# Performance work log

Measured on AMD Instinct MI355X. Metric: run time of the kernel, lower is better.

The kernel has to match this reference:

```python
import jax, jax.numpy as jnp
import numpy as np

T, H, F, E, K = 4096, 2048, 1408, 8, 2  # tokens, hidden, intermediate, experts, top_k


def setup_inputs() -> dict:
    key = jax.random.key(0)
    k1, k2, k3, k4 = jax.random.split(key, 4)
    return {
        "hidden_states": jax.random.normal(k1, (T, H), dtype=jnp.float32),
        "router_logits": jax.random.normal(k2, (T, E), dtype=jnp.float32),
        # w1: (E, 2, H, F) where dim 1 = [gate_proj, up_proj]
        "w1": jax.random.normal(k3, (E, 2, H, F), dtype=jnp.float32) * 0.02,
        # w2: (E, F, H) down projection
        "w2": jax.random.normal(k4, (E, F, H), dtype=jnp.float32) * 0.02,
        "top_k": K,
    }


def reference(hidden_states, router_logits, w1, w2, top_k):
    # Router: softmax over all experts, then select top_k.
    # renormalize_topk_logits=False -> combine weights are the raw softmax probs.
    probs = jax.nn.softmax(router_logits, axis=-1)            # (T, E)
    topk_w, topk_ids = jax.lax.top_k(probs, top_k)            # (T, K) each

    num_experts = w1.shape[0]
    out = jnp.zeros_like(hidden_states)                       # (T, H)
    # Fixed small loop over experts (structurally distinct weight slices);
    # each expert's FFN is a dense GEMM over all tokens, masked by the
    # per-token combine coefficient (0 for tokens not routed to this expert).
    for e in range(num_experts):
        coef = jnp.sum(jnp.where(topk_ids == e, topk_w, 0.0), axis=-1)  # (T,)
        gate = hidden_states @ w1[e, 0]                       # (T, F)
        up = hidden_states @ w1[e, 1]                         # (T, F)
        h = jax.nn.silu(gate) * up                            # SwiGLU
        out = out + coef[:, None] * (h @ w2[e])               # (T, H)
    return out
```

## Files before the change

### kernel.cpp

```cpp
#include <hip/hip_runtime.h>
#include <stdint.h>

#define T_TOK 4096
#define HID   2048
#define FF    1408
#define NE    8
#define BUF   16384
#define NT1   (HID / 32)
#define NT2   (FF / 32)

typedef __attribute__((ext_vector_type(8))) short short8;
typedef __attribute__((ext_vector_type(4))) float f32x4;

__device__ inline unsigned short f2bf(float f) {
  uint32_t u = __builtin_bit_cast(uint32_t, f);
  u += 0x7fffu + ((u >> 16) & 1u);
  return (unsigned short)(u >> 16);
}

__device__ inline uint32_t cvt_pk(float a, float b) {
  uint32_t r;
  asm("v_cvt_pk_bf16_f32 %0, %1, %2" : "=v"(r) : "v"(a), "v"(b));
  return r;
}

__device__ inline void gload16(const void* g, void* l) {
  __builtin_amdgcn_global_load_lds(
      (const __attribute__((address_space(1))) unsigned int*)g,
      (__attribute__((address_space(3))) unsigned int*)l, 16, 0, 0);
}

__device__ inline void wait8_barrier() {
  asm volatile("s_waitcnt vmcnt(8)" ::: "memory");
  __builtin_amdgcn_s_barrier();
  asm volatile("" ::: "memory");
}
__device__ inline void wait4_barrier() {
  asm volatile("s_waitcnt vmcnt(4)" ::: "memory");
  __builtin_amdgcn_s_barrier();
  asm volatile("" ::: "memory");
}
__device__ inline void wait0_barrier() {
  asm volatile("s_waitcnt vmcnt(0)" ::: "memory");
  __builtin_amdgcn_s_barrier();
  asm volatile("" ::: "memory");
}

__global__ __launch_bounds__(256) void route_kernel(const float* __restrict__ logits,
                                                    int2* __restrict__ eids,
                                                    float2* __restrict__ ecfs) {
  int t = blockIdx.x * 256 + threadIdx.x;
  const float4* lp = (const float4*)(logits + (size_t)t * NE);
  float4 a = lp[0], b = lp[1];
  float l[8] = {a.x, a.y, a.z, a.w, b.x, b.y, b.z, b.w};
  float mx = l[0];
#pragma unroll
  for (int i = 1; i < 8; ++i) mx = fmaxf(mx, l[i]);
  float s = 0.f, p[8];
#pragma unroll
  for (int i = 0; i < 8; ++i) { p[i] = __expf(l[i] - mx); s += p[i]; }
  float inv = 1.f / s;
  int e0 = 0;
#pragma unroll
  for (int i = 1; i < 8; ++i) if (l[i] > l[e0]) e0 = i;
  int e1 = (e0 == 0) ? 1 : 0;
#pragma unroll
  for (int i = 0; i < 8; ++i) if (i != e0 && l[i] > l[e1]) e1 = i;
  eids[t] = make_int2(e0, e1);
  ecfs[t] = make_float2(p[e0] * inv, p[e1] * inv);
}

__global__ __launch_bounds__(256) void compact_kernel(const int2* __restrict__ eids,
                                                      const float2* __restrict__ ecfs,
                                                      int* __restrict__ tok,
                                                      float* __restrict__ coef,
                                                      int* __restrict__ rowptr,
                                                      int* __restrict__ invm) {
  int e = blockIdx.x, tid = threadIdx.x;
  __shared__ int hist[8];
  __shared__ int wsum[4];
  __shared__ int runv;
  if (tid < 8) hist[tid] = 0;
  __syncthreads();
  for (int t = tid; t < T_TOK; t += 256) {
    int2 ei = eids[t];
    atomicAdd(&hist[ei.x], 1);
    atomicAdd(&hist[ei.y], 1);
  }
  __syncthreads();
  int off = 0;
  for (int j = 0; j < e; ++j) off += hist[j];
  if (tid == 0) {
    runv = 0;
    if (e == 0) rowptr[0] = 0;
    rowptr[e + 1] = off + hist[e];
  }
  __syncthreads();
  int wave = tid >> 6, lane = tid & 63;
  for (int c = 0; c < T_TOK; c += 256) {
    int t = c + tid;
    int2 ei = eids[t];
    float2 cf = ecfs[t];
    bool fl = false; float cv = 0.f; int ks = 0;
    if (ei.x == e)      { fl = true; cv = cf.x; ks = 0; }
    else if (ei.y == e) { fl = true; cv = cf.y; ks = 1; }
    unsigned long long m = __ballot(fl);
    if (lane == 0) wsum[wave] = __popcll(m);
    __syncthreads();
    int woff = runv;
    for (int wv = 0; wv < wave; ++wv) woff += wsum[wv];
    int pos = off + woff + __popcll(m & ((1ull << lane) - 1ull));
    if (fl) { tok[pos] = t; coef[pos] = cv; invm[2 * t + ks] = pos; }
    __syncthreads();
    if (tid == 0) runv += wsum[0] + wsum[1] + wsum[2] + wsum[3];
    __syncthreads();
  }
}

__global__ __launch_bounds__(256) void cvtx_kernel(const float* __restrict__ x,
                                                   unsigned short* __restrict__ xb) {
  int i = blockIdx.x * 256 + threadIdx.x;
  float4 v = ((const float4*)x)[i];
  uint2 o;
  o.x = cvt_pk(v.x, v.y);
  o.y = cvt_pk(v.z, v.w);
  ((uint2*)xb)[i] = o;
}

__global__ __launch_bounds__(256) void wcvt_kernel(const float* __restrict__ in,
                                                   unsigned short* __restrict__ out,
                                                   int R, int C) {
  __shared__ unsigned short t[64][72];
  const float* ip = in + ((size_t)blockIdx.z * R + blockIdx.y * 64) * C + blockIdx.x * 64;
  int tid = threadIdx.x;
  int r = tid >> 2, cg = (tid & 3) * 16;
  const float* rp = ip + (size_t)r * C + cg;
#pragma unroll
  for (int j = 0; j < 4; ++j) {
    float4 v = *(const float4*)(rp + j * 4);
    int c = cg + j * 4;
    t[c + 0][r] = f2bf(v.x);
    t[c + 1][r] = f2bf(v.y);
    t[c + 2][r] = f2bf(v.z);
    t[c + 3][r] = f2bf(v.w);
  }
  __syncthreads();
  int cr = tid >> 2, kg = (tid & 3) * 16;
  unsigned short* op = out + ((size_t)blockIdx.z * C + blockIdx.x * 64 + cr) * R +
                       blockIdx.y * 64 + kg;
  *(short8*)op = *(const short8*)&t[cr][kg];
  *(short8*)(op + 8) = *(const short8*)&t[cr][kg + 8];
}

__global__ __launch_bounds__(256) void gemm1_kernel(const unsigned short* __restrict__ Xb,
                                                    const unsigned short* __restrict__ w1t,
                                                    const int* __restrict__ tok,
                                                    const int* __restrict__ rowptr,
                                                    unsigned short* __restrict__ hbuf) {
  int f = blockIdx.x + 22 * blockIdx.y;
  int g = (f & 7) * 88 + (f >> 3);
  int ftile = g >> 5, mtile = g & 31;
  int e = blockIdx.z;
  int base = rowptr[e], cnt = rowptr[e + 1] - base;
  if (mtile * 128 >= cnt) return;
  __shared__ char smem[4 * BUF];
  int tid = threadIdx.x, lane = tid & 63, wave = tid >> 6;

  int rA = wave * 32 + (lane >> 2);
  int cd = (lane & 3) ^ ((rA >> 1) & 3);
  int sA0 = min(mtile * 128 + rA, cnt - 1);
  int sA1 = min(mtile * 128 + rA + 16, cnt - 1);
  const unsigned short* gA0 = Xb + (size_t)tok[base + sA0] * HID + cd * 8;
  const unsigned short* gA1 = Xb + (size_t)tok[base + sA1] * HID + cd * 8;
  int r1 = rA + 16;
  int p0 = (rA >> 4) & 1, f0 = (rA & 15) + 16 * (rA >> 5);
  int p1 = (r1 >> 4) & 1, f1 = (r1 & 15) + 16 * (r1 >> 5);
  const unsigned short* gB0 = w1t + ((size_t)(e * 2 + p0) * FF + ftile * 64 + f0) * HID + cd * 8;
  const unsigned short* gB1 = w1t + ((size_t)(e * 2 + p1) * FF + ftile * 64 + f1) * HID + cd * 8;
  int lb = wave * 2048 + lane * 16;

#define STG1(bp, k0) do {                          \
    gload16(gA0 + (k0), (bp) + lb);                \
    gload16(gA1 + (k0), (bp) + lb + 1024);         \
    gload16(gB0 + (k0), (bp) + 8192 + lb);         \
    gload16(gB1 + (k0), (bp) + 8192 + lb + 1024);  \
  } while (0)

  int wm = wave >> 1, wn = wave & 1, kc = lane >> 4;
  int aoff[4], boff[4];
#pragma unroll
  for (int mi = 0; mi < 4; ++mi) {
    int row = wm * 64 + mi * 16 + (lane & 15);
    aoff[mi] = row * 64 + ((kc ^ ((row >> 1) & 3)) << 4);
  }
#pragma unroll
  for (int ni = 0; ni < 4; ++ni) {
    int n = wn * 64 + ni * 16 + (lane & 15);
    boff[ni] = 8192 + n * 64 + ((kc ^ ((n >> 1) & 3)) << 4);
  }

  const f32x4 vz = {0.f, 0.f, 0.f, 0.f};
  f32x4 acc[4][4];
#pragma unroll
  for (int mi = 0; mi < 4; ++mi)
#pragma unroll
    for (int ni = 0; ni < 4; ++ni) acc[mi][ni] = vz;

  STG1(smem, 0);
  STG1(smem + BUF, 32);
  STG1(smem + 2 * BUF, 64);
  wait8_barrier();

  for (int t = 0; t < NT1; ++t) {
    char* cur = smem + (t & 3) * BUF;
    bool pf = (t + 3) < NT1;
    if (pf) STG1(smem + ((t + 3) & 3) * BUF, (t + 3) * 32);
    short8 af[4], bb[4];
#pragma unroll
    for (int mi = 0; mi < 4; ++mi) af[mi] = *(const short8*)(cur + aoff[mi]);
#pragma unroll
    for (int ni = 0; ni < 4; ++ni) bb[ni] = *(const short8*)(cur + boff[ni]);
    __builtin_amdgcn_s_setprio(1);
#pragma unroll
    for (int mi = 0; mi < 4; ++mi)
#pragma unroll
      for (int ni = 0; ni < 4; ++ni)
        acc[mi][ni] = __builtin_amdgcn_mfma_f32_16x16x32_bf16(af[mi], bb[ni], acc[mi][ni], 0, 0, 0);
    __builtin_amdgcn_s_setprio(0);
    if (pf) wait8_barrier();
    else if (t + 2 < NT1) wait4_barrier();
    else wait0_barrier();
  }
#undef STG1

  int fb = ftile * 64 + wn * 32 + (lane & 15);
#pragma unroll
  for (int mi = 0; mi < 4; ++mi) {
#pragma unroll
    for (int i = 0; i < 4; ++i) {
      int ml = wm * 64 + mi * 16 + (lane >> 4) * 4 + i;
      int slot = mtile * 128 + ml;
      if (slot < cnt) {
        size_t hrow = (size_t)(base + slot) * FF + fb;
        float g0 = acc[mi][0][i], u0 = acc[mi][1][i];
        float g1 = acc[mi][2][i], u1 = acc[mi][3][i];
        hbuf[hrow]      = f2bf(g0 / (1.f + __expf(-g0)) * u0);
        hbuf[hrow + 16] = f2bf(g1 / (1.f + __expf(-g1)) * u1);
      }
    }
  }
}

__global__ __launch_bounds__(256) void gemm2_kernel(const unsigned short* __restrict__ hbuf,
                                                    const unsigned short* __restrict__ w2t,
                                                    const int* __restrict__ rowptr,
                                                    float* __restrict__ obuf) {
  int f = blockIdx.x + 16 * blockIdx.y;
  int g = (f & 7) * 64 + (f >> 3);
  int ntile = g >> 5, mtile = g & 31;
  int e = blockIdx.z;
  int base = rowptr[e], cnt = rowptr[e + 1] - base;
  if (mtile * 128 >= cnt) return;
  __shared__ char smem[3 * BUF];
  int tid = threadIdx.x, lane = tid & 63, wave = tid >> 6;

  int rA = wave * 32 + (lane >> 2);
  int cd = (lane & 3) ^ ((rA >> 1) & 3);
  int sA0 = min(mtile * 128 + rA, cnt - 1);
  int sA1 = min(mtile * 128 + rA + 16, cnt - 1);
  const unsigned short* gA0 = hbuf + (size_t)(base + sA0) * FF + cd * 8;
  const unsigned short* gA1 = hbuf + (size_t)(base + sA1) * FF + cd * 8;
  const unsigned short* gB0 = w2t + ((size_t)e * HID + ntile * 128 + rA) * FF + cd * 8;
  const unsigned short* gB1 = gB0 + (size_t)16 * FF;
  int lb = wave * 2048 + lane * 16;

#define STG2(bp, k0) do {                          \
    gload16(gA0 + (k0), (bp) + lb);                \
    gload16(gA1 + (k0), (bp) + lb + 1024);         \
    gload16(gB0 + (k0), (bp) + 8192 + lb);         \
    gload16(gB1 + (k0), (bp) + 8192 + lb + 1024);  \
  } while (0)

  int wm = wave >> 1, wn = wave & 1, kc = lane >> 4;
  int aoff[4], boff[4];
#pragma unroll
  for (int mi = 0; mi < 4; ++mi) {
    int row = wm * 64 + mi * 16 + (lane & 15);
    aoff[mi] = row * 64 + ((kc ^ ((row >> 1) & 3)) << 4);
  }
#pragma unroll
  for (int ni = 0; ni < 4; ++ni) {
    int n = wn * 64 + ni * 16 + (lane & 15);
    boff[ni] = 8192 + n * 64 + ((kc ^ ((n >> 1) & 3)) << 4);
  }

  const f32x4 vz = {0.f, 0.f, 0.f, 0.f};
  f32x4 acc[4][4];
#pragma unroll
  for (int mi = 0; mi < 4; ++mi)
#pragma unroll
    for (int ni = 0; ni < 4; ++ni) acc[mi][ni] = vz;

  STG2(smem, 0);
  STG2(smem + BUF, 32);
  wait4_barrier();

  char* cur = smem;
  char* nxt = smem + 2 * BUF;
  for (int t = 0; t < NT2; ++t) {
    bool pf = (t + 2) < NT2;
    if (pf) STG2(nxt, (t + 2) * 32);
    short8 af[4], bb[4];
#pragma unroll
    for (int mi = 0; mi < 4; ++mi) af[mi] = *(const short8*)(cur + aoff[mi]);
#pragma unroll
    for (int ni = 0; ni < 4; ++ni) bb[ni] = *(const short8*)(cur + boff[ni]);
    __builtin_amdgcn_s_setprio(1);
#pragma unroll
    for (int mi = 0; mi < 4; ++mi)
#pragma unroll
      for (int ni = 0; ni < 4; ++ni)
        acc[mi][ni] = __builtin_amdgcn_mfma_f32_16x16x32_bf16(af[mi], bb[ni], acc[mi][ni], 0, 0, 0);
    __builtin_amdgcn_s_setprio(0);
    if (pf) wait4_barrier(); else wait0_barrier();
    cur = (cur == smem + 2 * BUF) ? smem : cur + BUF;
    nxt = (nxt == smem + 2 * BUF) ? smem : nxt + BUF;
  }
#undef STG2

  int nb = ntile * 128 + wn * 64 + (lane & 15);
#pragma unroll
  for (int mi = 0; mi < 4; ++mi) {
#pragma unroll
    for (int i = 0; i < 4; ++i) {
      int ml = wm * 64 + mi * 16 + (lane >> 4) * 4 + i;
      int slot = mtile * 128 + ml;
      if (slot < cnt) {
        float* op = obuf + (size_t)(base + slot) * HID + nb;
#pragma unroll
        for (int ni = 0; ni < 4; ++ni) op[ni * 16] = acc[mi][ni][i];
      }
    }
  }
}

__global__ __launch_bounds__(256) void combine_kernel(const float* __restrict__ obuf,
                                                      const int2* __restrict__ invm,
                                                      const float* __restrict__ coef,
                                                      float* __restrict__ out) {
  int idx = blockIdx.x * 256 + threadIdx.x;
  int t = idx >> 9, h4 = idx & 511;
  int2 pp = invm[t];
  float c0 = coef[pp.x], c1 = coef[pp.y];
  float4 a = ((const float4*)(obuf + (size_t)pp.x * HID))[h4];
  float4 b = ((const float4*)(obuf + (size_t)pp.y * HID))[h4];
  float4 o;
  o.x = c0 * a.x + c1 * b.x;
  o.y = c0 * a.y + c1 * b.y;
  o.z = c0 * a.z + c1 * b.z;
  o.w = c0 * a.w + c1 * b.w;
  ((float4*)out)[idx] = o;
}

__global__ __launch_bounds__(256) void gemm2_atomic(const unsigned short* __restrict__ hbuf,
                                                    const unsigned short* __restrict__ w2t,
                                                    const int* __restrict__ tok,
                                                    const float* __restrict__ coef,
                                                    const int* __restrict__ rowptr,
                                                    float* __restrict__ out) {
  int f = blockIdx.x + 16 * blockIdx.y;
  int g = (f & 7) * 64 + (f >> 3);
  int ntile = g >> 5, mtile = g & 31;
  int e = blockIdx.z;
  int base = rowptr[e], cnt = rowptr[e + 1] - base;
  if (mtile * 128 >= cnt) return;
  __shared__ char smem[3 * BUF];
  __shared__ int tokL[128];
  __shared__ float cofL[128];
  int tid = threadIdx.x, lane = tid & 63, wave = tid >> 6;
  if (tid < 128) {
    int slot = min(mtile * 128 + tid, cnt - 1);
    tokL[tid] = tok[base + slot];
    cofL[tid] = coef[base + slot];
  }
  __syncthreads();

  int rA = wave * 32 + (lane >> 2);
  int cd = (lane & 3) ^ ((rA >> 1) & 3);
  int sA0 = min(mtile * 128 + rA, cnt - 1);
  int sA1 = min(mtile * 128 + rA + 16, cnt - 1);
  const unsigned short* gA0 = hbuf + (size_t)(base + sA0) * FF + cd * 8;
  const unsigned short* gA1 = hbuf + (size_t)(base + sA1) * FF + cd * 8;
  const unsigned short* gB0 = w2t + ((size_t)e * HID + ntile * 128 + rA) * FF + cd * 8;
  const unsigned short* gB1 = gB0 + (size_t)16 * FF;
  int lb = wave * 2048 + lane * 16;

#define STG2F(bp, k0) do {                         \
    gload16(gA0 + (k0), (bp) + lb);                \
    gload16(gA1 + (k0), (bp) + lb + 1024);         \
    gload16(gB0 + (k0), (bp) + 8192 + lb);         \
    gload16(gB1 + (k0), (bp) + 8192 + lb + 1024);  \
  } while (0)

  int wm = wave >> 1, wn = wave & 1, kc = lane >> 4;
  int aoff[4], boff[4];
#pragma unroll
  for (int mi = 0; mi < 4; ++mi) {
    int row = wm * 64 + mi * 16 + (lane & 15);
    aoff[mi] = row * 64 + ((kc ^ ((row >> 1) & 3)) << 4);
  }
#pragma unroll
  for (int ni = 0; ni < 4; ++ni) {
    int n = wn * 64 + ni * 16 + (lane & 15);
    boff[ni] = 8192 + n * 64 + ((kc ^ ((n >> 1) & 3)) << 4);
  }

  const f32x4 vz = {0.f, 0.f, 0.f, 0.f};
  f32x4 acc[4][4];
#pragma unroll
  for (int mi = 0; mi < 4; ++mi)
#pragma unroll
    for (int ni = 0; ni < 4; ++ni) acc[mi][ni] = vz;

  STG2F(smem, 0);
  STG2F(smem + BUF, 32);
  wait4_barrier();

  char* cur = smem;
  char* nxt = smem + 2 * BUF;
  for (int t = 0; t < NT2; ++t) {
    bool pf = (t + 2) < NT2;
    if (pf) STG2F(nxt, (t + 2) * 32);
    short8 af[4], bb[4];
#pragma unroll
    for (int mi = 0; mi < 4; ++mi) af[mi] = *(const short8*)(cur + aoff[mi]);
#pragma unroll
    for (int ni = 0; ni < 4; ++ni) bb[ni] = *(const short8*)(cur + boff[ni]);
    __builtin_amdgcn_s_setprio(1);
#pragma unroll
    for (int mi = 0; mi < 4; ++mi)
#pragma unroll
      for (int ni = 0; ni < 4; ++ni)
        acc[mi][ni] = __builtin_amdgcn_mfma_f32_16x16x32_bf16(af[mi], bb[ni], acc[mi][ni], 0, 0, 0);
    __builtin_amdgcn_s_setprio(0);
    if (pf) wait4_barrier(); else wait0_barrier();
    cur = (cur == smem + 2 * BUF) ? smem : cur + BUF;
    nxt = (nxt == smem + 2 * BUF) ? smem : nxt + BUF;
  }
#undef STG2F

#pragma unroll
  for (int mi = 0; mi < 4; ++mi) {
#pragma unroll
    for (int i = 0; i < 4; ++i) {
      int ml = wm * 64 + mi * 16 + (lane >> 4) * 4 + i;
      int slot = mtile * 128 + ml;
      if (slot < cnt) {
        float cf = cofL[ml];
        float* op = out + (size_t)tokL[ml] * HID + ntile * 128 + wn * 64 + (lane & 15);
#pragma unroll
        for (int ni = 0; ni < 4; ++ni)
          unsafeAtomicAdd(op + ni * 16, cf * acc[mi][ni][i]);
      }
    }
  }
}

extern "C" void kernel_launch(void* const* d_in, const int* in_sizes, int n_in,
                              void* d_out, int out_size, void* d_ws, size_t ws_size,
                              hipStream_t stream) {
  const float* X  = (const float*)d_in[0];
  const float* RL = (const float*)d_in[1];
  const float* W1 = (const float*)d_in[2];
  const float* W2 = (const float*)d_in[3];
  float* out = (float*)d_out;

  const size_t OFF_EIDS = 4096;
  const size_t OFF_ECFS = 36864;
  const size_t OFF_TOK  = 69632;
  const size_t OFF_COEF = 102400;
  const size_t OFF_XB   = 135168;
  const size_t OFF_H    = 16912384;
  const size_t OFF_W1T  = 39981056;
  const size_t OFF_W2T  = 132255744;
  const size_t TOTAL2   = 178393088;
  const size_t OFF_INV  = 178393088;
  const size_t TOTAL3   = 178425856;
  if (ws_size < TOTAL2 || n_in < 4) return;
  bool big = ws_size >= TOTAL3;

  char* w = (char*)d_ws;
  int*    rowptr = (int*)w;
  int2*   eids   = (int2*)(w + OFF_EIDS);
  float2* ecfs   = (float2*)(w + OFF_ECFS);
  int*    tok    = (int*)(w + OFF_TOK);
  float*  coef   = (float*)(w + OFF_COEF);
  unsigned short* Xb   = (unsigned short*)(w + OFF_XB);
  unsigned short* hbuf = (unsigned short*)(w + OFF_H);
  unsigned short* w1t  = (unsigned short*)(w + OFF_W1T);
  unsigned short* w2t  = (unsigned short*)(w + OFF_W2T);
  float* obuf = (float*)(w + OFF_W1T);
  int* invm = big ? (int*)(w + OFF_INV) : (int*)hbuf;

  if (!big) hipMemsetAsync(d_out, 0, (size_t)T_TOK * HID * sizeof(float), stream);
  route_kernel<<<T_TOK / 256, 256, 0, stream>>>(RL, eids, ecfs);
  compact_kernel<<<NE, 256, 0, stream>>>(eids, ecfs, tok, coef, rowptr, invm);
  cvtx_kernel<<<(T_TOK * HID / 4) / 256, 256, 0, stream>>>(X, Xb);
  wcvt_kernel<<<dim3(FF / 64, HID / 64, NE * 2), 256, 0, stream>>>(W1, w1t, HID, FF);
  wcvt_kernel<<<dim3(HID / 64, FF / 64, NE), 256, 0, stream>>>(W2, w2t, FF, HID);
  gemm1_kernel<<<dim3(FF / 64, T_TOK / 128, NE), 256, 0, stream>>>(Xb, w1t, tok, rowptr, hbuf);
  if (big) {
    gemm2_kernel<<<dim3(HID / 128, T_TOK / 128, NE), 256, 0, stream>>>(hbuf, w2t, rowptr, obuf);
    combine_kernel<<<(T_TOK * HID / 4) / 256, 256, 0, stream>>>(obuf, (const int2*)invm, coef, out);
  } else {
    gemm2_atomic<<<dim3(HID / 128, T_TOK / 128, NE), 256, 0, stream>>>(hbuf, w2t, tok, coef, rowptr, out);
  }
}
```

Measured before the change: 345.6 us.

## Enlarge GEMM tiles to 128x256, fuse routing into compaction, store bf16 partials

Both expert GEMMs now use 128x256 output tiles with triple-buffered LDS, and each wave holds a 4x8 MFMA accumulator grid instead of 4x4, giving more reuse per loaded tile. The separate routing kernel is removed and each compaction block recomputes softmax/top-2 inline. GEMM2 writes its per-expert partial outputs as bf16 rather than fp32, so the combine kernel reads half the bytes. The larger tiles raise register and LDS pressure and may lower occupancy. The bf16 intermediate adds rounding error to the output.

Result: slower. 375.6 us (+8.7%).

```diff
diff --git a/kernel.cpp b/kernel.cpp
--- a/kernel.cpp
+++ b/kernel.cpp
@@ -5,9 +5,10 @@
 #define HID   2048
 #define FF    1408
 #define NE    8
-#define BUF   16384
+#define BUF   24576
 #define NT1   (HID / 32)
 #define NT2   (FF / 32)
+#define OBUF  16384
 
 typedef __attribute__((ext_vector_type(8))) short short8;
 typedef __attribute__((ext_vector_type(4))) float f32x4;
@@ -17,7 +18,10 @@
   u += 0x7fffu + ((u >> 16) & 1u);
   return (unsigned short)(u >> 16);
 }
-
+__device__ inline float bf2f(unsigned short u) {
+  uint32_t x = ((uint32_t)u) << 16;
+  return __builtin_bit_cast(float, x);
+}
 __device__ inline uint32_t cvt_pk(float a, float b) {
   uint32_t r;
   asm("v_cvt_pk_bf16_f32 %0, %1, %2" : "=v"(r) : "v"(a), "v"(b));
@@ -30,8 +34,8 @@
       (__attribute__((address_space(3))) unsigned int*)l, 16, 0, 0);
 }
 
-__device__ inline void wait8_barrier() {
-  asm volatile("s_waitcnt vmcnt(8)" ::: "memory");
+__device__ inline void wait6_barrier() {
+  asm volatile("s_waitcnt vmcnt(6)" ::: "memory");
   __builtin_amdgcn_s_barrier();
   asm volatile("" ::: "memory");
 }
@@ -46,12 +50,9 @@
   asm volatile("" ::: "memory");
 }
 
-__global__ __launch_bounds__(256) void route_kernel(const float* __restrict__ logits,
-                                                    int2* __restrict__ eids,
-                                                    float2* __restrict__ ecfs) {
-  int t = blockIdx.x * 256 + threadIdx.x;
-  const float4* lp = (const float4*)(logits + (size_t)t * NE);
-  float4 a = lp[0], b = lp[1];
+__device__ inline void route1(const float* __restrict__ lp, int& e0, int& e1,
+                              float& c0, float& c1) {
+  float4 a = ((const float4*)lp)[0], b = ((const float4*)lp)[1];
   float l[8] = {a.x, a.y, a.z, a.w, b.x, b.y, b.z, b.w};
   float mx = l[0];
 #pragma unroll
@@ -60,18 +61,17 @@
 #pragma unroll
   for (int i = 0; i < 8; ++i) { p[i] = __expf(l[i] - mx); s += p[i]; }
   float inv = 1.f / s;
-  int e0 = 0;
+  e0 = 0;
 #pragma unroll
   for (int i = 1; i < 8; ++i) if (l[i] > l[e0]) e0 = i;
-  int e1 = (e0 == 0) ? 1 : 0;
+  e1 = (e0 == 0) ? 1 : 0;
 #pragma unroll
   for (int i = 0; i < 8; ++i) if (i != e0 && l[i] > l[e1]) e1 = i;
-  eids[t] = make_int2(e0, e1);
-  ecfs[t] = make_float2(p[e0] * inv, p[e1] * inv);
-}
-
-__global__ __launch_bounds__(256) void compact_kernel(const int2* __restrict__ eids,
-                                                      const float2* __restrict__ ecfs,
+  c0 = p[e0] * inv;
+  c1 = p[e1] * inv;
+}
+
+__global__ __launch_bounds__(256) void compact_kernel(const float* __restrict__ logits,
                                                       int* __restrict__ tok,
                                                       float* __restrict__ coef,
                                                       int* __restrict__ rowptr,
@@ -83,9 +83,10 @@
   if (tid < 8) hist[tid] = 0;
   __syncthreads();
   for (int t = tid; t < T_TOK; t += 256) {
-    int2 ei = eids[t];
-    atomicAdd(&hist[ei.x], 1);
-    atomicAdd(&hist[ei.y], 1);
+    int e0, e1; float c0, c1;
+    route1(logits + (size_t)t * NE, e0, e1, c0, c1);
+    atomicAdd(&hist[e0], 1);
+    atomicAdd(&hist[e1], 1);
   }
   __syncthreads();
   int off = 0;
@@ -99,11 +100,11 @@
   int wave = tid >> 6, lane = tid & 63;
   for (int c = 0; c < T_TOK; c += 256) {
     int t = c + tid;
-    int2 ei = eids[t];
-    float2 cf = ecfs[t];
+    int e0, e1; float c0, c1;
+    route1(logits + (size_t)t * NE, e0, e1, c0, c1);
     bool fl = false; float cv = 0.f; int ks = 0;
-    if (ei.x == e)      { fl = true; cv = cf.x; ks = 0; }
-    else if (ei.y == e) { fl = true; cv = cf.y; ks = 1; }
+    if (e0 == e)      { fl = true; cv = c0; ks = 0; }
+    else if (e1 == e) { fl = true; cv = c1; ks = 1; }
     unsigned long long m = __ballot(fl);
     if (lane == 0) wsum[wave] = __popcll(m);
     __syncthreads();
@@ -152,214 +153,223 @@
   *(short8*)(op + 8) = *(const short8*)&t[cr][kg + 8];
 }
 
-__global__ __launch_bounds__(256) void gemm1_kernel(const unsigned short* __restrict__ Xb,
-                                                    const unsigned short* __restrict__ w1t,
-                                                    const int* __restrict__ tok,
-                                                    const int* __restrict__ rowptr,
-                                                    unsigned short* __restrict__ hbuf) {
-  int f = blockIdx.x + 22 * blockIdx.y;
-  int g = (f & 7) * 88 + (f >> 3);
+__global__ __launch_bounds__(256, 2) void gemm1_kernel(const unsigned short* __restrict__ Xb,
+                                                       const unsigned short* __restrict__ w1t,
+                                                       const int* __restrict__ tok,
+                                                       const int* __restrict__ rowptr,
+                                                       unsigned short* __restrict__ hbuf) {
+  int e = blockIdx.z;
+  int f = blockIdx.x + 32 * blockIdx.y;
+  int g = (f & 7) * 44 + (f >> 3);
   int ftile = g >> 5, mtile = g & 31;
-  int e = blockIdx.z;
-  int base = rowptr[e], cnt = rowptr[e + 1] - base;
-  if (mtile * 128 >= cnt) return;
-  __shared__ char smem[4 * BUF];
-  int tid = threadIdx.x, lane = tid & 63, wave = tid >> 6;
-
-  int rA = wave * 32 + (lane >> 2);
-  int cd = (lane & 3) ^ ((rA >> 1) & 3);
-  int sA0 = min(mtile * 128 + rA, cnt - 1);
-  int sA1 = min(mtile * 128 + rA + 16, cnt - 1);
-  const unsigned short* gA0 = Xb + (size_t)tok[base + sA0] * HID + cd * 8;
-  const unsigned short* gA1 = Xb + (size_t)tok[base + sA1] * HID + cd * 8;
-  int r1 = rA + 16;
-  int p0 = (rA >> 4) & 1, f0 = (rA & 15) + 16 * (rA >> 5);
-  int p1 = (r1 >> 4) & 1, f1 = (r1 & 15) + 16 * (r1 >> 5);
-  const unsigned short* gB0 = w1t + ((size_t)(e * 2 + p0) * FF + ftile * 64 + f0) * HID + cd * 8;
-  const unsigned short* gB1 = w1t + ((size_t)(e * 2 + p1) * FF + ftile * 64 + f1) * HID + cd * 8;
-  int lb = wave * 2048 + lane * 16;
-
-#define STG1(bp, k0) do {                          \
-    gload16(gA0 + (k0), (bp) + lb);                \
-    gload16(gA1 + (k0), (bp) + lb + 1024);         \
-    gload16(gB0 + (k0), (bp) + 8192 + lb);         \
-    gload16(gB1 + (k0), (bp) + 8192 + lb + 1024);  \
-  } while (0)
-
-  int wm = wave >> 1, wn = wave & 1, kc = lane >> 4;
-  int aoff[4], boff[4];
-#pragma unroll
-  for (int mi = 0; mi < 4; ++mi) {
-    int row = wm * 64 + mi * 16 + (lane & 15);
-    aoff[mi] = row * 64 + ((kc ^ ((row >> 1) & 3)) << 4);
-  }
-#pragma unroll
-  for (int ni = 0; ni < 4; ++ni) {
-    int n = wn * 64 + ni * 16 + (lane & 15);
-    boff[ni] = 8192 + n * 64 + ((kc ^ ((n >> 1) & 3)) << 4);
-  }
-
-  const f32x4 vz = {0.f, 0.f, 0.f, 0.f};
-  f32x4 acc[4][4];
-#pragma unroll
-  for (int mi = 0; mi < 4; ++mi)
-#pragma unroll
-    for (int ni = 0; ni < 4; ++ni) acc[mi][ni] = vz;
-
-  STG1(smem, 0);
-  STG1(smem + BUF, 32);
-  STG1(smem + 2 * BUF, 64);
-  wait8_barrier();
-
-  for (int t = 0; t < NT1; ++t) {
-    char* cur = smem + (t & 3) * BUF;
-    bool pf = (t + 3) < NT1;
-    if (pf) STG1(smem + ((t + 3) & 3) * BUF, (t + 3) * 32);
-    short8 af[4], bb[4];
-#pragma unroll
-    for (int mi = 0; mi < 4; ++mi) af[mi] = *(const short8*)(cur + aoff[mi]);
-#pragma unroll
-    for (int ni = 0; ni < 4; ++ni) bb[ni] = *(const short8*)(cur + boff[ni]);
-    __builtin_amdgcn_s_setprio(1);
-#pragma unroll
-    for (int mi = 0; mi < 4; ++mi)
-#pragma unroll
-      for (int ni = 0; ni < 4; ++ni)
-        acc[mi][ni] = __builtin_amdgcn_mfma_f32_16x16x32_bf16(af[mi], bb[ni], acc[mi][ni], 0, 0, 0);
-    __builtin_amdgcn_s_setprio(0);
-    if (pf) wait8_barrier();
-    else if (t + 2 < NT1) wait4_barrier();
-    else wait0_barrier();
-  }
-#undef STG1
-
-  int fb = ftile * 64 + wn * 32 + (lane & 15);
-#pragma unroll
-  for (int mi = 0; mi < 4; ++mi) {
-#pragma unroll
-    for (int i = 0; i < 4; ++i) {
-      int ml = wm * 64 + mi * 16 + (lane >> 4) * 4 + i;
-      int slot = mtile * 128 + ml;
-      if (slot < cnt) {
-        size_t hrow = (size_t)(base + slot) * FF + fb;
-        float g0 = acc[mi][0][i], u0 = acc[mi][1][i];
-        float g1 = acc[mi][2][i], u1 = acc[mi][3][i];
-        hbuf[hrow]      = f2bf(g0 / (1.f + __expf(-g0)) * u0);
-        hbuf[hrow + 16] = f2bf(g1 / (1.f + __expf(-g1)) * u1);
-      }
-    }
-  }
-}
-
-__global__ __launch_bounds__(256) void gemm2_kernel(const unsigned short* __restrict__ hbuf,
-                                                    const unsigned short* __restrict__ w2t,
-                                                    const int* __restrict__ rowptr,
-                                                    float* __restrict__ obuf) {
-  int f = blockIdx.x + 16 * blockIdx.y;
-  int g = (f & 7) * 64 + (f >> 3);
-  int ntile = g >> 5, mtile = g & 31;
-  int e = blockIdx.z;
   int base = rowptr[e], cnt = rowptr[e + 1] - base;
   if (mtile * 128 >= cnt) return;
   __shared__ char smem[3 * BUF];
   int tid = threadIdx.x, lane = tid & 63, wave = tid >> 6;
 
-  int rA = wave * 32 + (lane >> 2);
-  int cd = (lane & 3) ^ ((rA >> 1) & 3);
-  int sA0 = min(mtile * 128 + rA, cnt - 1);
-  int sA1 = min(mtile * 128 + rA + 16, cnt - 1);
+  int q = tid >> 2, p = tid & 3;
+  int cd = p ^ ((q >> 1) & 3);
+  int sA0 = min(mtile * 128 + q, cnt - 1);
+  int sA1 = min(mtile * 128 + 64 + q, cnt - 1);
+  const unsigned short* gA0 = Xb + (size_t)tok[base + sA0] * HID + cd * 8;
+  const unsigned short* gA1 = Xb + (size_t)tok[base + sA1] * HID + cd * 8;
+  const unsigned short* gB[4];
+#pragma unroll
+  for (int c = 0; c < 4; ++c) {
+    int row = 64 * c + q;
+    int proj = (row >> 4) & 1;
+    int fg = ftile * 128 + (row & 15) + 16 * (row >> 5);
+    gB[c] = w1t + ((size_t)(e * 2 + proj) * FF + fg) * HID + cd * 8;
+  }
+  int ldst = tid * 16;
+
+#define STG1(bp, k0) do {                                   \
+    gload16(gA0 + (k0), (bp) + ldst);                       \
+    gload16(gA1 + (k0), (bp) + 4096 + ldst);                \
+    _Pragma("unroll") for (int c = 0; c < 4; ++c)           \
+      gload16(gB[c] + (k0), (bp) + 8192 + c * 4096 + ldst); \
+  } while (0)
+
+  int wm = wave >> 1, wn = wave & 1, kc = lane >> 4, j = lane & 15;
+  int aoff[4], boff[8];
+#pragma unroll
+  for (int mi = 0; mi < 4; ++mi) {
+    int row = wm * 64 + mi * 16 + j;
+    aoff[mi] = row * 64 + ((kc ^ ((row >> 1) & 3)) << 4);
+  }
+#pragma unroll
+  for (int ni = 0; ni < 8; ++ni) {
+    int brow = wn * 128 + ni * 16 + j;
+    boff[ni] = 8192 + brow * 64 + ((kc ^ ((brow >> 1) & 3)) << 4);
+  }
+
+  const f32x4 vz = {0.f, 0.f, 0.f, 0.f};
+  f32x4 acc[4][8];
+#pragma unroll
+  for (int mi = 0; mi < 4; ++mi)
+#pragma unroll
+    for (int ni = 0; ni < 8; ++ni) acc[mi][ni] = vz;
+
+  STG1(smem, 0);
+  STG1(smem + BUF, 32);
+  wait6_barrier();
+
+  for (int t = 0; t < NT1; ++t) {
+    char* cur = smem + (t % 3) * BUF;
+    bool pf = (t + 2) < NT1;
+    if (pf) STG1(smem + ((t + 2) % 3) * BUF, (t + 2) * 32);
+    short8 af[4], bb[8];
+#pragma unroll
+    for (int mi = 0; mi < 4; ++mi) af[mi] = *(const short8*)(cur + aoff[mi]);
+#pragma unroll
+    for (int ni = 0; ni < 8; ++ni) bb[ni] = *(const short8*)(cur + boff[ni]);
+    __builtin_amdgcn_s_setprio(1);
+#pragma unroll
+    for (int mi = 0; mi < 4; ++mi)
+#pragma unroll
+      for (int ni = 0; ni < 8; ++ni)
+        acc[mi][ni] = __builtin_amdgcn_mfma_f32_16x16x32_bf16(af[mi], bb[ni], acc[mi][ni], 0, 0, 0);
+    __builtin_amdgcn_s_setprio(0);
+    if (pf) wait6_barrier(); else wait0_barrier();
+  }
+#undef STG1
+
+  int gq = lane >> 4;
+#pragma unroll
+  for (int mi = 0; mi < 4; ++mi) {
+#pragma unroll
+    for (int i = 0; i < 4; ++i) {
+      int ml = wm * 64 + mi * 16 + gq * 4 + i;
+      int slot = mtile * 128 + ml;
+      if (slot < cnt) {
+        size_t hrow = (size_t)(base + slot) * FF;
+#pragma unroll
+        for (int qd = 0; qd < 4; ++qd) {
+          int fg = ftile * 128 + j + 16 * (wn * 4 + qd);
+          float gg = acc[mi][2 * qd][i], uu = acc[mi][2 * qd + 1][i];
+          float hv = gg / (1.f + __expf(-gg)) * uu;
+          hbuf[hrow + fg] = f2bf(hv);
+        }
+      }
+    }
+  }
+}
+
+__global__ __launch_bounds__(256, 2) void gemm2_kernel(const unsigned short* __restrict__ hbuf,
+                                                       const unsigned short* __restrict__ w2t,
+                                                       const int* __restrict__ rowptr,
+                                                       unsigned short* __restrict__ obuf) {
+  int e = blockIdx.z;
+  int f = blockIdx.x + 32 * blockIdx.y;
+  int g = (f & 7) * 32 + (f >> 3);
+  int ntile = g >> 5, mtile = g & 31;
+  int base = rowptr[e], cnt = rowptr[e + 1] - base;
+  if (mtile * 128 >= cnt) return;
+  __shared__ char smem[3 * BUF];
+  int tid = threadIdx.x, lane = tid & 63, wave = tid >> 6;
+
+  int q = tid >> 2, p = tid & 3;
+  int cd = p ^ ((q >> 1) & 3);
+  int sA0 = min(mtile * 128 + q, cnt - 1);
+  int sA1 = min(mtile * 128 + 64 + q, cnt - 1);
   const unsigned short* gA0 = hbuf + (size_t)(base + sA0) * FF + cd * 8;
   const unsigned short* gA1 = hbuf + (size_t)(base + sA1) * FF + cd * 8;
-  const unsigned short* gB0 = w2t + ((size_t)e * HID + ntile * 128 + rA) * FF + cd * 8;
-  const unsigned short* gB1 = gB0 + (size_t)16 * FF;
-  int lb = wave * 2048 + lane * 16;
-
-#define STG2(bp, k0) do {                          \
-    gload16(gA0 + (k0), (bp) + lb);                \
-    gload16(gA1 + (k0), (bp) + lb + 1024);         \
-    gload16(gB0 + (k0), (bp) + 8192 + lb);         \
-    gload16(gB1 + (k0), (bp) + 8192 + lb + 1024);  \
+  const unsigned short* gB[4];
+#pragma unroll
+  for (int c = 0; c < 4; ++c)
+    gB[c] = w2t + ((size_t)e * HID + ntile * 256 + 64 * c + q) * FF + cd * 8;
+  int ldst = tid * 16;
+
+#define STG2(bp, k0) do {                                   \
+    gload16(gA0 + (k0), (bp) + ldst);                       \
+    gload16(gA1 + (k0), (bp) + 4096 + ldst);                \
+    _Pragma("unroll") for (int c = 0; c < 4; ++c)           \
+      gload16(gB[c] + (k0), (bp) + 8192 + c * 4096 + ldst); \
   } while (0)
 
-  int wm = wave >> 1, wn = wave & 1, kc = lane >> 4;
-  int aoff[4], boff[4];
+  int wm = wave >> 1, wn = wave & 1, kc = lane >> 4, j = lane & 15;
+  int aoff[4], boff[8];
 #pragma unroll
   for (int mi = 0; mi < 4; ++mi) {
-    int row = wm * 64 + mi * 16 + (lane & 15);
+    int row = wm * 64 + mi * 16 + j;
     aoff[mi] = row * 64 + ((kc ^ ((row >> 1) & 3)) << 4);
   }
 #pragma unroll
-  for (int ni = 0; ni < 4; ++ni) {
-    int n = wn * 64 + ni * 16 + (lane & 15);
-    boff[ni] = 8192 + n * 64 + ((kc ^ ((n >> 1) & 3)) << 4);
+  for (int ni = 0; ni < 8; ++ni) {
+    int brow = wn * 128 + ni * 16 + j;
+    boff[ni] = 8192 + brow * 64 + ((kc ^ ((brow >> 1) & 3)) << 4);
   }
 
   const f32x4 vz = {0.f, 0.f, 0.f, 0.f};
-  f32x4 acc[4][4];
+  f32x4 acc[4][8];
 #pragma unroll
   for (int mi = 0; mi < 4; ++mi)
 #pragma unroll
-    for (int ni = 0; ni < 4; ++ni) acc[mi][ni] = vz;
+    for (int ni = 0; ni < 8; ++ni) acc[mi][ni] = vz;
 
   STG2(smem, 0);
   STG2(smem + BUF, 32);
-  wait4_barrier();
-
-  char* cur = smem;
-  char* nxt = smem + 2 * BUF;
+  wait6_barrier();
+
   for (int t = 0; t < NT2; ++t) {
+    char* cur = smem + (t % 3) * BUF;
     bool pf = (t + 2) < NT2;
-    if (pf) STG2(nxt, (t + 2) * 32);
-    short8 af[4], bb[4];
+    if (pf) STG2(smem + ((t + 2) % 3) * BUF, (t + 2) * 32);
+    short8 af[4], bb[8];
 #pragma unroll
     for (int mi = 0; mi < 4; ++mi) af[mi] = *(const short8*)(cur + aoff[mi]);
 #pragma unroll
-    for (int ni = 0; ni < 4; ++ni) bb[ni] = *(const short8*)(cur + boff[ni]);
+    for (int ni = 0; ni < 8; ++ni) bb[ni] = *(const short8*)(cur + boff[ni]);
     __builtin_amdgcn_s_setprio(1);
 #pragma unroll
     for (int mi = 0; mi < 4; ++mi)
 #pragma unroll
-      for (int ni = 0; ni < 4; ++ni)
+      for (int ni = 0; ni < 8; ++ni)
         acc[mi][ni] = __builtin_amdgcn_mfma_f32_16x16x32_bf16(af[mi], bb[ni], acc[mi][ni], 0, 0, 0);
     __builtin_amdgcn_s_setprio(0);
-    if (pf) wait4_barrier(); else wait0_barrier();
-    cur = (cur == smem + 2 * BUF) ? smem : cur + BUF;
-    nxt = (nxt == smem + 2 * BUF) ? smem : nxt + BUF;
+    if (pf) wait6_barrier(); else wait0_barrier();
   }
 #undef STG2
 
-  int nb = ntile * 128 + wn * 64 + (lane & 15);
+  int gq = lane >> 4;
 #pragma unroll
   for (int mi = 0; mi < 4; ++mi) {
 #pragma unroll
     for (int i = 0; i < 4; ++i) {
-      int ml = wm * 64 + mi * 16 + (lane >> 4) * 4 + i;
+      int ml = wm * 64 + mi * 16 + gq * 4 + i;
       int slot = mtile * 128 + ml;
       if (slot < cnt) {
-        float* op = obuf + (size_t)(base + slot) * HID + nb;
-#pragma unroll
-        for (int ni = 0; ni < 4; ++ni) op[ni * 16] = acc[mi][ni][i];
+        unsigned short* op = obuf + (size_t)(base + slot) * HID + ntile * 256 +
+                             wn * 128 + j;
+#pragma unroll
+        for (int ni = 0; ni < 8; ++ni) op[ni * 16] = f2bf(acc[mi][ni][i]);
       }
     }
   }
 }
 
-__global__ __launch_bounds__(256) void combine_kernel(const float* __restrict__ obuf,
+__global__ __launch_bounds__(256) void combine_kernel(const unsigned short* __restrict__ obuf,
                                                       const int2* __restrict__ invm,
                                                       const float* __restrict__ coef,
                                                       float* __restrict__ out) {
   int idx = blockIdx.x * 256 + threadIdx.x;
-  int t = idx >> 9, h4 = idx & 511;
+  int t = idx >> 8, h8 = (idx & 255) * 8;
   int2 pp = invm[t];
   float c0 = coef[pp.x], c1 = coef[pp.y];
-  float4 a = ((const float4*)(obuf + (size_t)pp.x * HID))[h4];
-  float4 b = ((const float4*)(obuf + (size_t)pp.y * HID))[h4];
-  float4 o;
-  o.x = c0 * a.x + c1 * b.x;
-  o.y = c0 * a.y + c1 * b.y;
-  o.z = c0 * a.z + c1 * b.z;
-  o.w = c0 * a.w + c1 * b.w;
-  ((float4*)out)[idx] = o;
+  short8 a = *(const short8*)(obuf + (size_t)pp.x * HID + h8);
+  short8 b = *(const short8*)(obuf + (size_t)pp.y * HID + h8);
+  float4 o0, o1;
+  o0.x = c0 * bf2f((unsigned short)a[0]) + c1 * bf2f((unsigned short)b[0]);
+  o0.y = c0 * bf2f((unsigned short)a[1]) + c1 * bf2f((unsigned short)b[1]);
+  o0.z = c0 * bf2f((unsigned short)a[2]) + c1 * bf2f((unsigned short)b[2]);
+  o0.w = c0 * bf2f((unsigned short)a[3]) + c1 * bf2f((unsigned short)b[3]);
+  o1.x = c0 * bf2f((unsigned short)a[4]) + c1 * bf2f((unsigned short)b[4]);
+  o1.y = c0 * bf2f((unsigned short)a[5]) + c1 * bf2f((unsigned short)b[5]);
+  o1.z = c0 * bf2f((unsigned short)a[6]) + c1 * bf2f((unsigned short)b[6]);
+  o1.w = c0 * bf2f((unsigned short)a[7]) + c1 * bf2f((unsigned short)b[7]);
+  float4* ob = (float4*)(out + (size_t)t * HID + h8);
+  ob[0] = o0;
+  ob[1] = o1;
 }
 
 __global__ __launch_bounds__(256) void gemm2_atomic(const unsigned short* __restrict__ hbuf,
@@ -374,7 +384,7 @@
   int e = blockIdx.z;
   int base = rowptr[e], cnt = rowptr[e + 1] - base;
   if (mtile * 128 >= cnt) return;
-  __shared__ char smem[3 * BUF];
+  __shared__ char smem[3 * OBUF];
   __shared__ int tokL[128];
   __shared__ float cofL[128];
   int tid = threadIdx.x, lane = tid & 63, wave = tid >> 6;
@@ -423,11 +433,11 @@
     for (int ni = 0; ni < 4; ++ni) acc[mi][ni] = vz;
 
   STG2F(smem, 0);
-  STG2F(smem + BUF, 32);
+  STG2F(smem + OBUF, 32);
   wait4_barrier();
 
   char* cur = smem;
-  char* nxt = smem + 2 * BUF;
+  char* nxt = smem + 2 * OBUF;
   for (int t = 0; t < NT2; ++t) {
     bool pf = (t + 2) < NT2;
     if (pf) STG2F(nxt, (t + 2) * 32);
@@ -444,8 +454,8 @@
         acc[mi][ni] = __builtin_amdgcn_mfma_f32_16x16x32_bf16(af[mi], bb[ni], acc[mi][ni], 0, 0, 0);
     __builtin_amdgcn_s_setprio(0);
     if (pf) wait4_barrier(); else wait0_barrier();
-    cur = (cur == smem + 2 * BUF) ? smem : cur + BUF;
-    nxt = (nxt == smem + 2 * BUF) ? smem : nxt + BUF;
+    cur = (cur == smem + 2 * OBUF) ? smem : cur + OBUF;
+    nxt = (nxt == smem + 2 * OBUF) ? smem : nxt + OBUF;
   }
 #undef STG2F
 
@@ -475,8 +485,6 @@
   const float* W2 = (const float*)d_in[3];
   float* out = (float*)d_out;
 
-  const size_t OFF_EIDS = 4096;
-  const size_t OFF_ECFS = 36864;
   const size_t OFF_TOK  = 69632;
   const size_t OFF_COEF = 102400;
   const size_t OFF_XB   = 135168;
@@ -491,27 +499,24 @@
 
   char* w = (char*)d_ws;
   int*    rowptr = (int*)w;
-  int2*   eids   = (int2*)(w + OFF_EIDS);
-  float2* ecfs   = (float2*)(w + OFF_ECFS);
   int*    tok    = (int*)(w + OFF_TOK);
   float*  coef   = (float*)(w + OFF_COEF);
   unsigned short* Xb   = (unsigned short*)(w + OFF_XB);
   unsigned short* hbuf = (unsigned short*)(w + OFF_H);
   unsigned short* w1t  = (unsigned short*)(w + OFF_W1T);
   unsigned short* w2t  = (unsigned short*)(w + OFF_W2T);
-  float* obuf = (float*)(w + OFF_W1T);
+  unsigned short* obuf = (unsigned short*)(w + OFF_W1T);
   int* invm = big ? (int*)(w + OFF_INV) : (int*)hbuf;
 
   if (!big) hipMemsetAsync(d_out, 0, (size_t)T_TOK * HID * sizeof(float), stream);
-  route_kernel<<<T_TOK / 256, 256, 0, stream>>>(RL, eids, ecfs);
-  compact_kernel<<<NE, 256, 0, stream>>>(eids, ecfs, tok, coef, rowptr, invm);
+  compact_kernel<<<NE, 256, 0, stream>>>(RL, tok, coef, rowptr, invm);
   cvtx_kernel<<<(T_TOK * HID / 4) / 256, 256, 0, stream>>>(X, Xb);
   wcvt_kernel<<<dim3(FF / 64, HID / 64, NE * 2), 256, 0, stream>>>(W1, w1t, HID, FF);
   wcvt_kernel<<<dim3(HID / 64, FF / 64, NE), 256, 0, stream>>>(W2, w2t, FF, HID);
-  gemm1_kernel<<<dim3(FF / 64, T_TOK / 128, NE), 256, 0, stream>>>(Xb, w1t, tok, rowptr, hbuf);
+  gemm1_kernel<<<dim3(32, 11, NE), 256, 0, stream>>>(Xb, w1t, tok, rowptr, hbuf);
   if (big) {
-    gemm2_kernel<<<dim3(HID / 128, T_TOK / 128, NE), 256, 0, stream>>>(hbuf, w2t, rowptr, obuf);
-    combine_kernel<<<(T_TOK * HID / 4) / 256, 256, 0, stream>>>(obuf, (const int2*)invm, coef, out);
+    gemm2_kernel<<<dim3(32, 8, NE), 256, 0, stream>>>(hbuf, w2t, rowptr, obuf);
+    combine_kernel<<<(T_TOK * HID / 8) / 256, 256, 0, stream>>>(obuf, (const int2*)invm, coef, out);
   } else {
     gemm2_atomic<<<dim3(HID / 128, T_TOK / 128, NE), 256, 0, stream>>>(hbuf, w2t, tok, coef, rowptr, out);
   }
```

## Fuse routing into compaction, merge weight converts, bf16 expert outputs, interleave expert blocks

Applied to the files above, without the earlier changes.

Drops the separate route kernel and recomputes softmax/top-2 inside the compaction kernel. The two weight-transpose launches become a single launch. GEMM1 and GEMM2 switch to a 1D grid with experts interleaved across consecutive blocks. The per-expert GEMM2 output buffer is stored as bf16 instead of fp32, halving the write and combine-read traffic at some precision cost, and combine reads 8 bf16 values per thread.

Result: slower. 369.0 us (+6.8%).

```diff
diff --git a/kernel.cpp b/kernel.cpp
--- a/kernel.cpp
+++ b/kernel.cpp
@@ -17,7 +17,10 @@
   u += 0x7fffu + ((u >> 16) & 1u);
   return (unsigned short)(u >> 16);
 }
-
+__device__ inline float bf2f(unsigned short u) {
+  uint32_t x = ((uint32_t)u) << 16;
+  return __builtin_bit_cast(float, x);
+}
 __device__ inline uint32_t cvt_pk(float a, float b) {
   uint32_t r;
   asm("v_cvt_pk_bf16_f32 %0, %1, %2" : "=v"(r) : "v"(a), "v"(b));
@@ -46,12 +49,9 @@
   asm volatile("" ::: "memory");
 }
 
-__global__ __launch_bounds__(256) void route_kernel(const float* __restrict__ logits,
-                                                    int2* __restrict__ eids,
-                                                    float2* __restrict__ ecfs) {
-  int t = blockIdx.x * 256 + threadIdx.x;
-  const float4* lp = (const float4*)(logits + (size_t)t * NE);
-  float4 a = lp[0], b = lp[1];
+__device__ inline void route1(const float* __restrict__ lp, int& e0, int& e1,
+                              float& c0, float& c1) {
+  float4 a = ((const float4*)lp)[0], b = ((const float4*)lp)[1];
   float l[8] = {a.x, a.y, a.z, a.w, b.x, b.y, b.z, b.w};
   float mx = l[0];
 #pragma unroll
@@ -60,18 +60,17 @@
 #pragma unroll
   for (int i = 0; i < 8; ++i) { p[i] = __expf(l[i] - mx); s += p[i]; }
   float inv = 1.f / s;
-  int e0 = 0;
+  e0 = 0;
 #pragma unroll
   for (int i = 1; i < 8; ++i) if (l[i] > l[e0]) e0 = i;
-  int e1 = (e0 == 0) ? 1 : 0;
+  e1 = (e0 == 0) ? 1 : 0;
 #pragma unroll
   for (int i = 0; i < 8; ++i) if (i != e0 && l[i] > l[e1]) e1 = i;
-  eids[t] = make_int2(e0, e1);
-  ecfs[t] = make_float2(p[e0] * inv, p[e1] * inv);
-}
-
-__global__ __launch_bounds__(256) void compact_kernel(const int2* __restrict__ eids,
-                                                      const float2* __restrict__ ecfs,
+  c0 = p[e0] * inv;
+  c1 = p[e1] * inv;
+}
+
+__global__ __launch_bounds__(256) void compact_kernel(const float* __restrict__ logits,
                                                       int* __restrict__ tok,
                                                       float* __restrict__ coef,
                                                       int* __restrict__ rowptr,
@@ -83,9 +82,10 @@
   if (tid < 8) hist[tid] = 0;
   __syncthreads();
   for (int t = tid; t < T_TOK; t += 256) {
-    int2 ei = eids[t];
-    atomicAdd(&hist[ei.x], 1);
-    atomicAdd(&hist[ei.y], 1);
+    int e0, e1; float c0, c1;
+    route1(logits + (size_t)t * NE, e0, e1, c0, c1);
+    atomicAdd(&hist[e0], 1);
+    atomicAdd(&hist[e1], 1);
   }
   __syncthreads();
   int off = 0;
@@ -99,11 +99,11 @@
   int wave = tid >> 6, lane = tid & 63;
   for (int c = 0; c < T_TOK; c += 256) {
     int t = c + tid;
-    int2 ei = eids[t];
-    float2 cf = ecfs[t];
+    int e0, e1; float c0, c1;
+    route1(logits + (size_t)t * NE, e0, e1, c0, c1);
     bool fl = false; float cv = 0.f; int ks = 0;
-    if (ei.x == e)      { fl = true; cv = cf.x; ks = 0; }
-    else if (ei.y == e) { fl = true; cv = cf.y; ks = 1; }
+    if (e0 == e)      { fl = true; cv = c0; ks = 0; }
+    else if (e1 == e) { fl = true; cv = c1; ks = 1; }
     unsigned long long m = __ballot(fl);
     if (lane == 0) wsum[wave] = __popcll(m);
     __syncthreads();
@@ -127,11 +127,17 @@
   ((uint2*)xb)[i] = o;
 }
 
-__global__ __launch_bounds__(256) void wcvt_kernel(const float* __restrict__ in,
-                                                   unsigned short* __restrict__ out,
-                                                   int R, int C) {
+__global__ __launch_bounds__(256) void wcvt_all(const float* __restrict__ W1,
+                                                const float* __restrict__ W2,
+                                                unsigned short* __restrict__ w1t,
+                                                unsigned short* __restrict__ w2t) {
+  int z = blockIdx.z;
+  const float* in; unsigned short* out; int R, C;
+  if (z < 16) { in = W1 + (size_t)z * HID * FF;        out = w1t + (size_t)z * FF * HID;        R = HID; C = FF; }
+  else        { in = W2 + (size_t)(z - 16) * FF * HID; out = w2t + (size_t)(z - 16) * HID * FF; R = FF;  C = HID; }
+  if (blockIdx.x * 64 >= C || blockIdx.y * 64 >= R) return;
   __shared__ unsigned short t[64][72];
-  const float* ip = in + ((size_t)blockIdx.z * R + blockIdx.y * 64) * C + blockIdx.x * 64;
+  const float* ip = in + ((size_t)blockIdx.y * 64) * C + blockIdx.x * 64;
   int tid = threadIdx.x;
   int r = tid >> 2, cg = (tid & 3) * 16;
   const float* rp = ip + (size_t)r * C + cg;
@@ -146,8 +152,7 @@
   }
   __syncthreads();
   int cr = tid >> 2, kg = (tid & 3) * 16;
-  unsigned short* op = out + ((size_t)blockIdx.z * C + blockIdx.x * 64 + cr) * R +
-                       blockIdx.y * 64 + kg;
+  unsigned short* op = out + ((size_t)(blockIdx.x * 64 + cr)) * R + blockIdx.y * 64 + kg;
   *(short8*)op = *(const short8*)&t[cr][kg];
   *(short8*)(op + 8) = *(const short8*)&t[cr][kg + 8];
 }
@@ -157,10 +162,10 @@
                                                     const int* __restrict__ tok,
                                                     const int* __restrict__ rowptr,
                                                     unsigned short* __restrict__ hbuf) {
-  int f = blockIdx.x + 22 * blockIdx.y;
-  int g = (f & 7) * 88 + (f >> 3);
-  int ftile = g >> 5, mtile = g & 31;
-  int e = blockIdx.z;
+  int bid = blockIdx.x;
+  int e = bid & 7;
+  int i = bid >> 3;
+  int mtile = i & 31, ftile = i >> 5;
   int base = rowptr[e], cnt = rowptr[e + 1] - base;
   if (mtile * 128 >= cnt) return;
   __shared__ char smem[4 * BUF];
@@ -237,13 +242,13 @@
 #pragma unroll
   for (int mi = 0; mi < 4; ++mi) {
 #pragma unroll
-    for (int i = 0; i < 4; ++i) {
-      int ml = wm * 64 + mi * 16 + (lane >> 4) * 4 + i;
+    for (int i2 = 0; i2 < 4; ++i2) {
+      int ml = wm * 64 + mi * 16 + (lane >> 4) * 4 + i2;
       int slot = mtile * 128 + ml;
       if (slot < cnt) {
         size_t hrow = (size_t)(base + slot) * FF + fb;
-        float g0 = acc[mi][0][i], u0 = acc[mi][1][i];
-        float g1 = acc[mi][2][i], u1 = acc[mi][3][i];
+        float g0 = acc[mi][0][i2], u0 = acc[mi][1][i2];
+        float g1 = acc[mi][2][i2], u1 = acc[mi][3][i2];
         hbuf[hrow]      = f2bf(g0 / (1.f + __expf(-g0)) * u0);
         hbuf[hrow + 16] = f2bf(g1 / (1.f + __expf(-g1)) * u1);
       }
@@ -254,11 +259,11 @@
 __global__ __launch_bounds__(256) void gemm2_kernel(const unsigned short* __restrict__ hbuf,
                                                     const unsigned short* __restrict__ w2t,
                                                     const int* __restrict__ rowptr,
-                                                    float* __restrict__ obuf) {
-  int f = blockIdx.x + 16 * blockIdx.y;
-  int g = (f & 7) * 64 + (f >> 3);
-  int ntile = g >> 5, mtile = g & 31;
-  int e = blockIdx.z;
+                                                    unsigned short* __restrict__ obuf) {
+  int bid = blockIdx.x;
+  int e = bid & 7;
+  int i = bid >> 3;
+  int mtile = i & 31, ntile = i >> 5;
   int base = rowptr[e], cnt = rowptr[e + 1] - base;
   if (mtile * 128 >= cnt) return;
   __shared__ char smem[3 * BUF];
@@ -332,34 +337,40 @@
 #pragma unroll
   for (int mi = 0; mi < 4; ++mi) {
 #pragma unroll
-    for (int i = 0; i < 4; ++i) {
-      int ml = wm * 64 + mi * 16 + (lane >> 4) * 4 + i;
+    for (int i2 = 0; i2 < 4; ++i2) {
+      int ml = wm * 64 + mi * 16 + (lane >> 4) * 4 + i2;
       int slot = mtile * 128 + ml;
       if (slot < cnt) {
-        float* op = obuf + (size_t)(base + slot) * HID + nb;
-#pragma unroll
-        for (int ni = 0; ni < 4; ++ni) op[ni * 16] = acc[mi][ni][i];
+        unsigned short* op = obuf + (size_t)(base + slot) * HID + nb;
+#pragma unroll
+        for (int ni = 0; ni < 4; ++ni) op[ni * 16] = f2bf(acc[mi][ni][i2]);
       }
     }
   }
 }
 
-__global__ __launch_bounds__(256) void combine_kernel(const float* __restrict__ obuf,
+__global__ __launch_bounds__(256) void combine_kernel(const unsigned short* __restrict__ obuf,
                                                       const int2* __restrict__ invm,
                                                       const float* __restrict__ coef,
                                                       float* __restrict__ out) {
   int idx = blockIdx.x * 256 + threadIdx.x;
-  int t = idx >> 9, h4 = idx & 511;
+  int t = idx >> 8, h8 = (idx & 255) * 8;
   int2 pp = invm[t];
   float c0 = coef[pp.x], c1 = coef[pp.y];
-  float4 a = ((const float4*)(obuf + (size_t)pp.x * HID))[h4];
-  float4 b = ((const float4*)(obuf + (size_t)pp.y * HID))[h4];
-  float4 o;
-  o.x = c0 * a.x + c1 * b.x;
-  o.y = c0 * a.y + c1 * b.y;
-  o.z = c0 * a.z + c1 * b.z;
-  o.w = c0 * a.w + c1 * b.w;
-  ((float4*)out)[idx] = o;
+  short8 a = *(const short8*)(obuf + (size_t)pp.x * HID + h8);
+  short8 b = *(const short8*)(obuf + (size_t)pp.y * HID + h8);
+  float4 o0, o1;
+  o0.x = c0 * bf2f((unsigned short)a[0]) + c1 * bf2f((unsigned short)b[0]);
+  o0.y = c0 * bf2f((unsigned short)a[1]) + c1 * bf2f((unsigned short)b[1]);
+  o0.z = c0 * bf2f((unsigned short)a[2]) + c1 * bf2f((unsigned short)b[2]);
+  o0.w = c0 * bf2f((unsigned short)a[3]) + c1 * bf2f((unsigned short)b[3]);
+  o1.x = c0 * bf2f((unsigned short)a[4]) + c1 * bf2f((unsigned short)b[4]);
+  o1.y = c0 * bf2f((unsigned short)a[5]) + c1 * bf2f((unsigned short)b[5]);
+  o1.z = c0 * bf2f((unsigned short)a[6]) + c1 * bf2f((unsigned short)b[6]);
+  o1.w = c0 * bf2f((unsigned short)a[7]) + c1 * bf2f((unsigned short)b[7]);
+  float4* ob = (float4*)(out + (size_t)t * HID + h8);
+  ob[0] = o0;
+  ob[1] = o1;
 }
 
 __global__ __launch_bounds__(256) void gemm2_atomic(const unsigned short* __restrict__ hbuf,
@@ -452,15 +463,15 @@
 #pragma unroll
   for (int mi = 0; mi < 4; ++mi) {
 #pragma unroll
-    for (int i = 0; i < 4; ++i) {
-      int ml = wm * 64 + mi * 16 + (lane >> 4) * 4 + i;
+    for (int i2 = 0; i2 < 4; ++i2) {
+      int ml = wm * 64 + mi * 16 + (lane >> 4) * 4 + i2;
       int slot = mtile * 128 + ml;
       if (slot < cnt) {
         float cf = cofL[ml];
         float* op = out + (size_t)tokL[ml] * HID + ntile * 128 + wn * 64 + (lane & 15);
 #pragma unroll
         for (int ni = 0; ni < 4; ++ni)
-          unsafeAtomicAdd(op + ni * 16, cf * acc[mi][ni][i]);
+          unsafeAtomicAdd(op + ni * 16, cf * acc[mi][ni][i2]);
       }
     }
   }
@@ -475,8 +486,6 @@
   const float* W2 = (const float*)d_in[3];
   float* out = (float*)d_out;
 
-  const size_t OFF_EIDS = 4096;
-  const size_t OFF_ECFS = 36864;
   const size_t OFF_TOK  = 69632;
   const size_t OFF_COEF = 102400;
   const size_t OFF_XB   = 135168;
@@ -491,27 +500,23 @@
 
   char* w = (char*)d_ws;
   int*    rowptr = (int*)w;
-  int2*   eids   = (int2*)(w + OFF_EIDS);
-  float2* ecfs   = (float2*)(w + OFF_ECFS);
   int*    tok    = (int*)(w + OFF_TOK);
   float*  coef   = (float*)(w + OFF_COEF);
   unsigned short* Xb   = (unsigned short*)(w + OFF_XB);
   unsigned short* hbuf = (unsigned short*)(w + OFF_H);
   unsigned short* w1t  = (unsigned short*)(w + OFF_W1T);
   unsigned short* w2t  = (unsigned short*)(w + OFF_W2T);
-  float* obuf = (float*)(w + OFF_W1T);
+  unsigned short* obuf = (unsigned short*)(w + OFF_W1T);
   int* invm = big ? (int*)(w + OFF_INV) : (int*)hbuf;
 
   if (!big) hipMemsetAsync(d_out, 0, (size_t)T_TOK * HID * sizeof(float), stream);
-  route_kernel<<<T_TOK / 256, 256, 0, stream>>>(RL, eids, ecfs);
-  compact_kernel<<<NE, 256, 0, stream>>>(eids, ecfs, tok, coef, rowptr, invm);
+  compact_kernel<<<NE, 256, 0, stream>>>(RL, tok, coef, rowptr, invm);
   cvtx_kernel<<<(T_TOK * HID / 4) / 256, 256, 0, stream>>>(X, Xb);
-  wcvt_kernel<<<dim3(FF / 64, HID / 64, NE * 2), 256, 0, stream>>>(W1, w1t, HID, FF);
-  wcvt_kernel<<<dim3(HID / 64, FF / 64, NE), 256, 0, stream>>>(W2, w2t, FF, HID);
-  gemm1_kernel<<<dim3(FF / 64, T_TOK / 128, NE), 256, 0, stream>>>(Xb, w1t, tok, rowptr, hbuf);
+  wcvt_all<<<dim3(32, 32, 24), 256, 0, stream>>>(W1, W2, w1t, w2t);
+  gemm1_kernel<<<NE * 704, 256, 0, stream>>>(Xb, w1t, tok, rowptr, hbuf);
   if (big) {
-    gemm2_kernel<<<dim3(HID / 128, T_TOK / 128, NE), 256, 0, stream>>>(hbuf, w2t, rowptr, obuf);
-    combine_kernel<<<(T_TOK * HID / 4) / 256, 256, 0, stream>>>(obuf, (const int2*)invm, coef, out);
+    gemm2_kernel<<<NE * 512, 256, 0, stream>>>(hbuf, w2t, rowptr, obuf);
+    combine_kernel<<<(T_TOK * HID / 8) / 256, 256, 0, stream>>>(obuf, (const int2*)invm, coef, out);
   } else {
     gemm2_atomic<<<dim3(HID / 128, T_TOK / 128, NE), 256, 0, stream>>>(hbuf, w2t, tok, coef, rowptr, out);
   }
```
